# Optimization experiments

Measured on AMD Instinct MI355X. Metric: run time of the kernel, lower is better.

The kernel has to match this reference:

```python
import jax, jax.numpy as jnp
import numpy as np
from jax import lax

LBDA = 0.1
EPS = 0.01
NUM_CLASSES = 20


def setup_inputs() -> dict:
    key = jax.random.key(0)
    k1, k2 = jax.random.split(key)
    target_features = jax.random.normal(k1, (2048, 8, 2048), dtype=jnp.float32)
    support_features = jax.random.normal(k2, (100, 8, 2048), dtype=jnp.float32)
    # 20-way 5-shot: every class present so per-class mean is well defined
    support_labels = jnp.repeat(jnp.arange(NUM_CLASSES, dtype=jnp.int32), 100 // NUM_CLASSES)
    return {
        "target_features": target_features,
        "support_features": support_features,
        "support_labels": support_labels,
    }


def _softmin(xs, lbda):
    # -lbda * log(sum_i exp(-x_i/lbda)), stable
    return -lbda * jax.nn.logsumexp(jnp.stack([-x / lbda for x in xs], axis=0), axis=0)


def otam_cum_dist(dists, lbda=LBDA):
    # dists: [Q, Sp, L, S] frame distance matrices
    d = jnp.pad(dists, ((0, 0), (0, 0), (0, 0), (1, 1)))  # pad columns -> M = S + 2
    M = d.shape[-1]
    # row 0: running sum along columns (cum[0,0] = d[0,0] = 0 from padding)
    row0 = jnp.cumsum(d[:, :, 0, :], axis=-1)

    def step(prev_row, d_row):
        # prev_row, d_row: [Q, Sp, M]; column 0 is never written -> stays 0
        cur = [jnp.zeros_like(d_row[..., 0])]
        cur.append(d_row[..., 1] + _softmin([prev_row[..., 0], prev_row[..., 1], cur[0]], lbda))
        for m in range(2, M - 1):
            cur.append(d_row[..., m] + _softmin([prev_row[..., m - 1], cur[m - 1]], lbda))
        cur.append(d_row[..., M - 1] + _softmin([prev_row[..., M - 2], prev_row[..., M - 1], cur[M - 2]], lbda))
        new_row = jnp.stack(cur, axis=-1)
        return new_row, None

    d_rows = jnp.moveaxis(d[:, :, 1:, :], 2, 0)  # [L-1, Q, Sp, M]
    final_row, _ = lax.scan(step, row0, d_rows)
    return final_row[..., -1]  # [Q, Sp]


def cos_sim(x, y, eps=EPS):
    num = x @ y.T
    den = jnp.linalg.norm(x, axis=-1)[:, None] * jnp.linalg.norm(y, axis=-1)[None, :] + eps
    return num / den


def reference(target_features, support_features, support_labels):
    Q, S, D = target_features.shape
    Sp = support_features.shape[0]
    tf = target_features.reshape(Q * S, D)
    sf = support_features.reshape(Sp * S, D)
    frame_dists = 1.0 - cos_sim(tf, sf)  # [Q*S, Sp*S]
    # '(tb ts) (sb ss) -> tb sb ts ss'
    dists = frame_dists.reshape(Q, S, Sp, S).transpose(0, 2, 1, 3)
    cum_dists = otam_cum_dist(dists) + otam_cum_dist(dists.transpose(0, 1, 3, 2))  # [Q, Sp]
    # per-class mean over support (torch.unique returns sorted labels 0..C-1)
    onehot = (support_labels[:, None] == jnp.arange(NUM_CLASSES)[None, :]).astype(cum_dists.dtype)
    onehot = onehot / jnp.sum(onehot, axis=0, keepdims=True)
    class_dists = cum_dists @ onehot  # [Q, C]
    return -class_dists[None]  # logits [1, Q, C]
```

## Files before the change

kernel.cpp:

```cpp
#include <hip/hip_runtime.h>

#define QN    2048
#define SS    8
#define DD    2048
#define SP    100
#define NCLS  20
#define MROWS (QN*SS)
#define NROWS (SP*SS)
#define NPAD  896
#define KK    DD

typedef __bf16 bf16x8 __attribute__((ext_vector_type(8)));
typedef float  f32x4  __attribute__((ext_vector_type(4)));

__device__ __forceinline__ unsigned short f2bf(float f) {
    unsigned int u = __float_as_uint(f);
    u += 0x7fffu + ((u >> 16) & 1u);
    return (unsigned short)(u >> 16);
}

__global__ void cvt_kernel(const float* __restrict__ tf, const float* __restrict__ sf,
                           unsigned short* __restrict__ Abf, unsigned short* __restrict__ Bbf,
                           float* __restrict__ nA, float* __restrict__ nB)
{
    const int wv   = threadIdx.x >> 6;
    const int lane = threadIdx.x & 63;
    const int row  = blockIdx.x * 4 + wv;

    const float* src = nullptr;
    unsigned short* dst;
    float* nrm; int r;
    if (row < MROWS) { src = tf + (size_t)row * DD; dst = Abf + (size_t)row * DD; nrm = nA; r = row; }
    else {
        r = row - MROWS;
        dst = Bbf + (size_t)r * DD; nrm = nB;
        if (r < NROWS) src = sf + (size_t)r * DD;
    }

    float s = 0.f;
#pragma unroll
    for (int j = 0; j < 8; j++) {
        ushort4 pk = make_ushort4(0, 0, 0, 0);
        if (src) {
            float4 v = *(const float4*)(src + j * 256 + lane * 4);
            s += v.x*v.x + v.y*v.y + v.z*v.z + v.w*v.w;
            pk = make_ushort4(f2bf(v.x), f2bf(v.y), f2bf(v.z), f2bf(v.w));
        }
        *(ushort4*)(dst + j * 256 + lane * 4) = pk;
    }
#pragma unroll
    for (int o = 32; o; o >>= 1) s += __shfl_down(s, o);
    if (lane == 0) nrm[r] = sqrtf(s);
}

__device__ __forceinline__ float softmin2(float a, float b) {
    float mn = fminf(a, b), mx = fmaxf(a, b);
    return mn - 0.1f * __logf(1.0f + __expf((mn - mx) * 10.0f));
}
__device__ __forceinline__ float softmin3(float a, float b, float c) {
    float mn = fminf(fminf(a, b), c);
    float sum = __expf((mn - a) * 10.0f) + __expf((mn - b) * 10.0f) + __expf((mn - c) * 10.0f);
    return mn - 0.1f * __logf(sum);
}

__device__ __forceinline__ void gld16(const void* g, void* l) {
    __builtin_amdgcn_global_load_lds(
        (const __attribute__((address_space(1))) unsigned int*)g,
        (__attribute__((address_space(3))) unsigned int*)l, 16, 0, 0);
}

__device__ __forceinline__ float cellf(const uint4* raw, int a, int b) {
    const unsigned* p = (const unsigned*)raw;
    unsigned wv = p[a * 4 + (b >> 1)];
    return __uint_as_float((b & 1) ? (wv & 0xffff0000u) : (wv << 16));
}

#define EBS (32 * 72)

__global__ __launch_bounds__(256, 2) void gemm_kernel(
    const unsigned short* __restrict__ A,
    const unsigned short* __restrict__ B,
    const float* __restrict__ nA, const float* __restrict__ nB,
    float* __restrict__ cum)
{
    __shared__ __align__(16) unsigned short smem[4 * EBS];
    unsigned short* Als = smem;
    unsigned short* Bls = smem + 4096;

    const int mt  = blockIdx.x;
    const int nt  = blockIdx.y;
    const int tid = threadIdx.x;
    const int lane = tid & 63;
    const int w    = tid >> 6;
    const int wm   = (w & 1) * 64, wn = (w >> 1) * 64;
    const int col  = lane & 15, kg = lane >> 4;

    f32x4 acc[4][4] = {};

    const int c0 = tid, c1 = tid + 256;
    const unsigned short* Ab0 = A + (size_t)(mt * 128 + (c0 >> 2)) * KK + (c0 & 3) * 8;
    const unsigned short* Ab1 = A + (size_t)(mt * 128 + (c1 >> 2)) * KK + (c1 & 3) * 8;
    const unsigned short* Bb0 = B + (size_t)(nt * 128 + (c0 >> 2)) * KK + (c0 & 3) * 8;
    const unsigned short* Bb1 = B + (size_t)(nt * 128 + (c1 >> 2)) * KK + (c1 & 3) * 8;

    for (int kk = 0; kk < KK; kk += 32) {
        __syncthreads();
        gld16(Ab0 + kk, (char*)Als + c0 * 16);
        gld16(Ab1 + kk, (char*)Als + c1 * 16);
        gld16(Bb0 + kk, (char*)Bls + c0 * 16);
        gld16(Bb1 + kk, (char*)Bls + c1 * 16);
        __syncthreads();
        bf16x8 af[4], bfr[4];
#pragma unroll
        for (int i = 0; i < 4; i++) af[i]  = *(const bf16x8*)(Als + (wm + i * 16 + col) * 32 + kg * 8);
#pragma unroll
        for (int i = 0; i < 4; i++) bfr[i] = *(const bf16x8*)(Bls + (wn + i * 16 + col) * 32 + kg * 8);
#pragma unroll
        for (int mi = 0; mi < 4; mi++)
#pragma unroll
            for (int ni = 0; ni < 4; ni++)
                acc[mi][ni] = __builtin_amdgcn_mfma_f32_16x16x32_bf16(af[mi], bfr[ni], acc[mi][ni], 0, 0, 0);
    }

    __syncthreads();

    unsigned short* eb = smem + w * EBS;
    const int mbase = mt * 128 + wm;
    const int nbase = nt * 128 + wn;
    const int pr  = lane & 31;
    const int qv2 = pr >> 3, sv = pr & 7;
    const int dir = lane >> 5;

#pragma unroll
    for (int p = 0; p < 2; p++) {
        if (p) __syncthreads();
#pragma unroll
        for (int mi2 = 0; mi2 < 2; mi2++) {
            const int mi = p * 2 + mi2;
            float nx[4];
#pragma unroll
            for (int r = 0; r < 4; r++) nx[r] = nA[mbase + mi * 16 + kg * 4 + r];
#pragma unroll
            for (int ni = 0; ni < 4; ni++) {
                const float ny = nB[nbase + ni * 16 + col];
#pragma unroll
                for (int r = 0; r < 4; r++) {
                    float d = 1.0f - acc[mi][ni][r] * __builtin_amdgcn_rcpf(nx[r] * ny + 0.01f);
                    eb[(mi2 * 16 + kg * 4 + r) * 72 + ni * 16 + col] = f2bf(d);
                }
            }
        }
        __syncthreads();

        uint4 raw[8];
        const unsigned short* tb = eb + (qv2 * 8) * 72 + sv * 8;
#pragma unroll
        for (int l = 0; l < 8; l++) raw[l] = *(const uint4*)(tb + l * 72);

        float prev[10], cur[10];
        prev[0] = 0.f;
#pragma unroll
        for (int m = 1; m <= 8; m++) {
            float v0 = cellf(raw, 0, m - 1), v1 = cellf(raw, m - 1, 0);
            prev[m] = prev[m - 1] + (dir ? v1 : v0);
        }
        prev[9] = prev[8];
#pragma unroll
        for (int l = 1; l < 8; l++) {
            float d[8];
#pragma unroll
            for (int j = 0; j < 8; j++) {
                float v0 = cellf(raw, l, j), v1 = cellf(raw, j, l);
                d[j] = dir ? v1 : v0;
            }
            cur[1] = d[0] + softmin3(prev[0], prev[1], 0.0f);
#pragma unroll
            for (int m = 2; m <= 8; m++)
                cur[m] = d[m - 1] + softmin2(prev[m - 1], cur[m - 1]);
            cur[9] = softmin3(prev[8], prev[9], cur[8]);
#pragma unroll
            for (int m = 1; m < 10; m++) prev[m] = cur[m];
        }
        float res = prev[9];
        res += __shfl_down(res, 32);
        if (dir == 0) {
            const int qg = mt * 16 + (wm >> 3) + p * 4 + qv2;
            const int sg = nt * 16 + (wn >> 3) + sv;
            if (sg < SP) cum[(size_t)qg * SP + sg] = res;
        }
    }
}

__global__ void cls_kernel(const float* __restrict__ cum, const int* __restrict__ labels,
                           float* __restrict__ out)
{
    int idx = blockIdx.x * 256 + threadIdx.x;
    int q = idx / NCLS, c = idx % NCLS;
    float s = 0.f; int n = 0;
    const float* row = cum + (size_t)q * SP;
    for (int sp = 0; sp < SP; sp++) {
        if (labels[sp] == c) { s += row[sp]; n++; }
    }
    out[idx] = -s / (float)n;
}

extern "C" void kernel_launch(void* const* d_in, const int* in_sizes, int n_in,
                              void* d_out, int out_size, void* d_ws, size_t ws_size,
                              hipStream_t stream)
{
    const float* tf     = (const float*)d_in[0];
    const float* sf     = (const float*)d_in[1];
    const int*   labels = (const int*)d_in[2];
    float* out = (float*)d_out;

    char* ws = (char*)d_ws;
    const size_t szA    = (size_t)MROWS * KK * 2;
    const size_t szB    = (size_t)NPAD  * KK * 2;
    const size_t szNA   = (size_t)MROWS * 4;
    const size_t szNB   = (size_t)NPAD  * 4;
    unsigned short* Abf = (unsigned short*)ws;
    unsigned short* Bbf = (unsigned short*)(ws + szA);
    float* nA   = (float*)(ws + szA + szB);
    float* nB   = (float*)(ws + szA + szB + szNA);
    float* cum  = (float*)(ws + szA + szB + szNA + szNB);

    cvt_kernel<<<(MROWS + NPAD) / 4, 256, 0, stream>>>(tf, sf, Abf, Bbf, nA, nB);
    gemm_kernel<<<dim3(MROWS / 128, NPAD / 128), 256, 0, stream>>>(Abf, Bbf, nA, nB, cum);
    cls_kernel<<<160, 256, 0, stream>>>(cum, labels, out);
}
```

Baseline: 317.4 us.

## Split GEMM into full and half-width tiles, fuse class mean via atomics

Reduces the padded support dimension from 896 to 832 rows. The last partial N tile is handled by a separate 128x64 kernel, so the wasted MFMA work on padding shrinks. The class-mean kernel is removed: each support result is atomically added, pre-scaled by 1/5, into the zeroed output. Launch bounds are raised to 4 blocks per CU. This adds a memset and atomic contention, hardcodes 5 shots per class, and the higher occupancy target may force register spills with the 64-float accumulator.

New measurement: 315.2 us. No clear change (-0.7%).

```diff
diff --git a/kernel.cpp b/kernel.cpp
--- a/kernel.cpp
+++ b/kernel.cpp
@@ -7,7 +7,7 @@
 #define NCLS  20
 #define MROWS (QN*SS)
 #define NROWS (SP*SS)
-#define NPAD  896
+#define NPAD  832
 #define KK    DD
 
 typedef __bf16 bf16x8 __attribute__((ext_vector_type(8)));
@@ -75,13 +75,42 @@
     return __uint_as_float((b & 1) ? (wv & 0xffff0000u) : (wv << 16));
 }
 
+__device__ __forceinline__ float otam_dp(const uint4* raw, int dir) {
+    float prev[10], cur[10];
+    prev[0] = 0.f;
+#pragma unroll
+    for (int m = 1; m <= 8; m++) {
+        float v0 = cellf(raw, 0, m - 1), v1 = cellf(raw, m - 1, 0);
+        prev[m] = prev[m - 1] + (dir ? v1 : v0);
+    }
+    prev[9] = prev[8];
+#pragma unroll
+    for (int l = 1; l < 8; l++) {
+        float d[8];
+#pragma unroll
+        for (int j = 0; j < 8; j++) {
+            float v0 = cellf(raw, l, j), v1 = cellf(raw, j, l);
+            d[j] = dir ? v1 : v0;
+        }
+        cur[1] = d[0] + softmin3(prev[0], prev[1], 0.0f);
+#pragma unroll
+        for (int m = 2; m <= 8; m++)
+            cur[m] = d[m - 1] + softmin2(prev[m - 1], cur[m - 1]);
+        cur[9] = softmin3(prev[8], prev[9], cur[8]);
+#pragma unroll
+        for (int m = 1; m < 10; m++) prev[m] = cur[m];
+    }
+    return prev[9];
+}
+
 #define EBS (32 * 72)
 
-__global__ __launch_bounds__(256, 2) void gemm_kernel(
+__global__ __launch_bounds__(256, 4) void gemm_full(
     const unsigned short* __restrict__ A,
     const unsigned short* __restrict__ B,
     const float* __restrict__ nA, const float* __restrict__ nB,
-    float* __restrict__ cum)
+    const int* __restrict__ labels,
+    float* __restrict__ out)
 {
     __shared__ __align__(16) unsigned short smem[4 * EBS];
     unsigned short* Als = smem;
@@ -157,51 +186,99 @@
 #pragma unroll
         for (int l = 0; l < 8; l++) raw[l] = *(const uint4*)(tb + l * 72);
 
-        float prev[10], cur[10];
-        prev[0] = 0.f;
-#pragma unroll
-        for (int m = 1; m <= 8; m++) {
-            float v0 = cellf(raw, 0, m - 1), v1 = cellf(raw, m - 1, 0);
-            prev[m] = prev[m - 1] + (dir ? v1 : v0);
-        }
-        prev[9] = prev[8];
-#pragma unroll
-        for (int l = 1; l < 8; l++) {
-            float d[8];
-#pragma unroll
-            for (int j = 0; j < 8; j++) {
-                float v0 = cellf(raw, l, j), v1 = cellf(raw, j, l);
-                d[j] = dir ? v1 : v0;
-            }
-            cur[1] = d[0] + softmin3(prev[0], prev[1], 0.0f);
-#pragma unroll
-            for (int m = 2; m <= 8; m++)
-                cur[m] = d[m - 1] + softmin2(prev[m - 1], cur[m - 1]);
-            cur[9] = softmin3(prev[8], prev[9], cur[8]);
-#pragma unroll
-            for (int m = 1; m < 10; m++) prev[m] = cur[m];
-        }
-        float res = prev[9];
+        float res = otam_dp(raw, dir);
         res += __shfl_down(res, 32);
         if (dir == 0) {
             const int qg = mt * 16 + (wm >> 3) + p * 4 + qv2;
             const int sg = nt * 16 + (wn >> 3) + sv;
-            if (sg < SP) cum[(size_t)qg * SP + sg] = res;
-        }
-    }
-}
-
-__global__ void cls_kernel(const float* __restrict__ cum, const int* __restrict__ labels,
-                           float* __restrict__ out)
+            if (sg < SP) atomicAdd(out + (size_t)qg * NCLS + labels[sg], -res * 0.2f);
+        }
+    }
+}
+
+#define EBH (64 * 40)
+
+__global__ __launch_bounds__(256, 4) void gemm_half(
+    const unsigned short* __restrict__ A,
+    const unsigned short* __restrict__ B,
+    const float* __restrict__ nA, const float* __restrict__ nB,
+    const int* __restrict__ labels,
+    float* __restrict__ out)
 {
-    int idx = blockIdx.x * 256 + threadIdx.x;
-    int q = idx / NCLS, c = idx % NCLS;
-    float s = 0.f; int n = 0;
-    const float* row = cum + (size_t)q * SP;
-    for (int sp = 0; sp < SP; sp++) {
-        if (labels[sp] == c) { s += row[sp]; n++; }
-    }
-    out[idx] = -s / (float)n;
+    __shared__ __align__(16) unsigned short smem[4 * EBH];
+    unsigned short* Als = smem;
+    unsigned short* Bls = smem + 4096;
+
+    const int mt  = blockIdx.x;
+    const int tid = threadIdx.x;
+    const int lane = tid & 63;
+    const int w    = tid >> 6;
+    const int wm   = (w & 1) * 64, wn = (w >> 1) * 32;
+    const int col  = lane & 15, kg = lane >> 4;
+
+    f32x4 acc[4][2] = {};
+
+    const int c0 = tid, c1 = tid + 256;
+    const unsigned short* Ab0 = A + (size_t)(mt * 128 + (c0 >> 2)) * KK + (c0 & 3) * 8;
+    const unsigned short* Ab1 = A + (size_t)(mt * 128 + (c1 >> 2)) * KK + (c1 & 3) * 8;
+    const unsigned short* Bb0 = B + (size_t)(768 + (c0 >> 2)) * KK + (c0 & 3) * 8;
+
+    for (int kk = 0; kk < KK; kk += 32) {
+        __syncthreads();
+        gld16(Ab0 + kk, (char*)Als + c0 * 16);
+        gld16(Ab1 + kk, (char*)Als + c1 * 16);
+        gld16(Bb0 + kk, (char*)Bls + c0 * 16);
+        __syncthreads();
+        bf16x8 af[4], bfr[2];
+#pragma unroll
+        for (int i = 0; i < 4; i++) af[i]  = *(const bf16x8*)(Als + (wm + i * 16 + col) * 32 + kg * 8);
+#pragma unroll
+        for (int i = 0; i < 2; i++) bfr[i] = *(const bf16x8*)(Bls + (wn + i * 16 + col) * 32 + kg * 8);
+#pragma unroll
+        for (int mi = 0; mi < 4; mi++)
+#pragma unroll
+            for (int ni = 0; ni < 2; ni++)
+                acc[mi][ni] = __builtin_amdgcn_mfma_f32_16x16x32_bf16(af[mi], bfr[ni], acc[mi][ni], 0, 0, 0);
+    }
+
+    __syncthreads();
+
+    unsigned short* eb = smem + w * EBH;
+    const int mbase = mt * 128 + wm;
+    const int nbase = 768 + wn;
+
+#pragma unroll
+    for (int mi = 0; mi < 4; mi++) {
+        float nx[4];
+#pragma unroll
+        for (int r = 0; r < 4; r++) nx[r] = nA[mbase + mi * 16 + kg * 4 + r];
+#pragma unroll
+        for (int ni = 0; ni < 2; ni++) {
+            const float ny = nB[nbase + ni * 16 + col];
+#pragma unroll
+            for (int r = 0; r < 4; r++) {
+                float d = 1.0f - acc[mi][ni][r] * __builtin_amdgcn_rcpf(nx[r] * ny + 0.01f);
+                eb[(mi * 16 + kg * 4 + r) * 40 + ni * 16 + col] = f2bf(d);
+            }
+        }
+    }
+    __syncthreads();
+
+    const int pr  = lane & 31;
+    const int qv  = pr >> 2, sv = pr & 3;
+    const int dir = lane >> 5;
+    uint4 raw[8];
+    const unsigned short* tb = eb + (qv * 8) * 40 + sv * 8;
+#pragma unroll
+    for (int l = 0; l < 8; l++) raw[l] = *(const uint4*)(tb + l * 40);
+
+    float res = otam_dp(raw, dir);
+    res += __shfl_down(res, 32);
+    if (dir == 0) {
+        const int qg = mt * 16 + (wm >> 3) + qv;
+        const int sg = 96 + (wn >> 3) + sv;
+        if (sg < SP) atomicAdd(out + (size_t)qg * NCLS + labels[sg], -res * 0.2f);
+    }
 }
 
 extern "C" void kernel_launch(void* const* d_in, const int* in_sizes, int n_in,
@@ -217,14 +294,13 @@
     const size_t szA    = (size_t)MROWS * KK * 2;
     const size_t szB    = (size_t)NPAD  * KK * 2;
     const size_t szNA   = (size_t)MROWS * 4;
-    const size_t szNB   = (size_t)NPAD  * 4;
     unsigned short* Abf = (unsigned short*)ws;
     unsigned short* Bbf = (unsigned short*)(ws + szA);
     float* nA   = (float*)(ws + szA + szB);
     float* nB   = (float*)(ws + szA + szB + szNA);
-    float* cum  = (float*)(ws + szA + szB + szNA + szNB);
-
+
+    hipMemsetAsync(out, 0, (size_t)QN * NCLS * sizeof(float), stream);
     cvt_kernel<<<(MROWS + NPAD) / 4, 256, 0, stream>>>(tf, sf, Abf, Bbf, nA, nB);
-    gemm_kernel<<<dim3(MROWS / 128, NPAD / 128), 256, 0, stream>>>(Abf, Bbf, nA, nB, cum);
-    cls_kernel<<<160, 256, 0, stream>>>(cum, labels, out);
-}
+    gemm_full<<<dim3(MROWS / 128, 6), 256, 0, stream>>>(Abf, Bbf, nA, nB, labels, out);
+    gemm_half<<<MROWS / 128, 256, 0, stream>>>(Abf, Bbf, nA, nB, labels, out);
+}
```
